# Performance work log

Measured on AMD Instinct MI355X. Metric: run time of the kernel, lower is better.

## Reference

```python
import jax, jax.numpy as jnp
import numpy as np

N_NODES = 100000
N_EDGES = 1600000
EDGES_IN = 1
HID = 64
OUT = 64


def setup_inputs() -> dict:
    key = jax.random.key(0)
    ks = jax.random.split(key, 10)
    s = lambda fan_in: 1.0 / np.sqrt(fan_in)
    inp = {
        "edge_index": jax.random.randint(ks[0], (2, N_EDGES), 0, N_NODES, dtype=jnp.int64) if jax.config.jax_enable_x64 else jax.random.randint(ks[0], (2, N_EDGES), 0, N_NODES, dtype=jnp.int32),
        "edge_attr": jax.random.normal(ks[1], (N_EDGES, EDGES_IN), dtype=jnp.float32),
        # edge MLP: Linear(EDGES_IN->HID), SiLU, Linear(HID->HID), SiLU
        "W1": jax.random.uniform(ks[2], (EDGES_IN, HID), jnp.float32, -s(EDGES_IN), s(EDGES_IN)),
        "b1": jax.random.uniform(ks[3], (HID,), jnp.float32, -s(EDGES_IN), s(EDGES_IN)),
        "W2": jax.random.uniform(ks[4], (HID, HID), jnp.float32, -s(HID), s(HID)),
        "b2": jax.random.uniform(ks[5], (HID,), jnp.float32, -s(HID), s(HID)),
        # node MLP: Linear(HID->HID), SiLU, Linear(HID->OUT)
        "W3": jax.random.uniform(ks[6], (HID, HID), jnp.float32, -s(HID), s(HID)),
        "b3": jax.random.uniform(ks[7], (HID,), jnp.float32, -s(HID), s(HID)),
        "W4": jax.random.uniform(ks[8], (HID, OUT), jnp.float32, -s(HID), s(HID)),
        "b4": jax.random.uniform(ks[9], (OUT,), jnp.float32, -s(HID), s(HID)),
    }
    return inp


def reference(edge_index, edge_attr, W1, b1, W2, b2, W3, b3, W4, b4):
    silu = jax.nn.silu
    # edge model: [E, EDGES_IN] -> [E, HID]
    ef = silu(edge_attr @ W1 + b1)
    ef = silu(ef @ W2 + b2)
    # unsorted_segment_sum over source nodes (row): [E, HID] -> [N, HID]
    row = edge_index[0]
    agg = jax.ops.segment_sum(ef, row, num_segments=N_NODES)
    # node model: [N, HID] -> [N, OUT]
    h = silu(agg @ W3 + b3) @ W4 + b4
    return h
```

## Files before the change

kernel.cpp:

```cpp
#include <hip/hip_runtime.h>
#include <math.h>
#include <utility>

#define TN 4096
#define XMIN (-8.0f)
#define XMAX (8.0f)

#define GB1 256
#define MAXBK 1024
#define S2_ELEMS 2048
#define S2_BS 256
#define BKN 128
#define BKCAP 3072

typedef __attribute__((ext_vector_type(8))) short short8;
typedef __attribute__((ext_vector_type(4))) float f32x4;

__device__ __forceinline__ float silu_f(float v) {
    return v / (1.0f + __expf(-v));
}

__device__ __forceinline__ unsigned short f2bf(float x) {
    unsigned u = __float_as_uint(x);
    return (unsigned short)((u + 0x7FFFu + ((u >> 16) & 1u)) >> 16);
}
__device__ __forceinline__ float bf2f(unsigned short h) {
    return __uint_as_float(((unsigned)h) << 16);
}

#define SPLIT8(w0,w1,w2,w3,w4,w5,w6,w7, H, L) { \
    unsigned short _h0=f2bf(w0),_h1=f2bf(w1),_h2=f2bf(w2),_h3=f2bf(w3), \
                   _h4=f2bf(w4),_h5=f2bf(w5),_h6=f2bf(w6),_h7=f2bf(w7); \
    H = (short8){(short)_h0,(short)_h1,(short)_h2,(short)_h3, \
                 (short)_h4,(short)_h5,(short)_h6,(short)_h7}; \
    L = (short8){(short)f2bf((w0)-bf2f(_h0)),(short)f2bf((w1)-bf2f(_h1)), \
                 (short)f2bf((w2)-bf2f(_h2)),(short)f2bf((w3)-bf2f(_h3)), \
                 (short)f2bf((w4)-bf2f(_h4)),(short)f2bf((w5)-bf2f(_h5)), \
                 (short)f2bf((w6)-bf2f(_h6)),(short)f2bf((w7)-bf2f(_h7))}; }

#define BFRAG(Wp, kc, nt, H, L) { \
    const float* _p = (Wp) + ((kc)*32 + quad*8)*64 + (nt)*16 + m; \
    SPLIT8(_p[0],_p[64],_p[128],_p[192],_p[256],_p[320],_p[384],_p[448], H, L) }

#define MFMA3(AH, AL, BH, BL, ACC) \
    ACC = __builtin_amdgcn_mfma_f32_16x16x32_bf16(AH, BH, ACC, 0, 0, 0); \
    ACC = __builtin_amdgcn_mfma_f32_16x16x32_bf16(AL, BH, ACC, 0, 0, 0); \
    ACC = __builtin_amdgcn_mfma_f32_16x16x32_bf16(AH, BL, ACC, 0, 0, 0);

__global__ void build_table_k(const float* __restrict__ W1, const float* __restrict__ b1,
                              const float* __restrict__ W2, const float* __restrict__ b2,
                              float* __restrict__ table) {
    int gid  = blockIdx.x * blockDim.x + threadIdx.x;
    int wave = gid >> 6;
    int lane = gid & 63;
    if (wave >= TN) return;
    const float step = (XMAX - XMIN) / (float)(TN - 1);
    float x  = XMIN + step * (float)wave;
    float h1 = silu_f(fmaf(x, W1[lane], b1[lane]));
    float acc = b2[lane];
#pragma unroll
    for (int k = 0; k < 64; ++k) {
        float h1k = __shfl(h1, k, 64);
        acc = fmaf(h1k, W2[k * 64 + lane], acc);
    }
    table[wave * 64 + lane] = silu_f(acc);
}

__global__ void bhist_k(const int* __restrict__ row, int* __restrict__ bh,
                        int E, int nbk) {
    __shared__ int h[MAXBK];
    int t = threadIdx.x;
    for (int e = t; e < nbk; e += 256) h[e] = 0;
    __syncthreads();
    for (int i = blockIdx.x * 256 + t; i < E; i += 256 * GB1)
        atomicAdd(&h[row[i] >> 7], 1);
    __syncthreads();
    for (int e = t; e < nbk; e += 256)
        bh[e * GB1 + blockIdx.x] = h[e];
}

__global__ void scan2A_k(const int* __restrict__ in, int* __restrict__ out,
                         int* __restrict__ bsum, int n) {
    __shared__ int b0[S2_ELEMS], b1[S2_ELEMS];
    int t = threadIdx.x, base = blockIdx.x * S2_ELEMS;
    for (int e = t; e < S2_ELEMS; e += S2_BS)
        b0[e] = (base + e < n) ? in[base + e] : 0;
    __syncthreads();
    int* src = b0; int* dst = b1;
    for (int d = 1; d < S2_ELEMS; d <<= 1) {
        for (int e = t; e < S2_ELEMS; e += S2_BS)
            dst[e] = src[e] + ((e >= d) ? src[e - d] : 0);
        __syncthreads();
        int* tmp = src; src = dst; dst = tmp;
    }
    for (int e = t; e < S2_ELEMS; e += S2_BS)
        if (base + e < n) out[base + e] = (e == 0) ? 0 : src[e - 1];
    if (t == 0) bsum[blockIdx.x] = src[S2_ELEMS - 1];
}

__global__ void scanB_k(int* __restrict__ bsum, int nb) {
    __shared__ int b0[256], b1[256];
    int t = threadIdx.x;
    b0[t] = (t < nb) ? bsum[t] : 0;
    __syncthreads();
    int* src = b0; int* dst = b1;
    for (int d = 1; d < 256; d <<= 1) {
        dst[t] = src[t] + ((t >= d) ? src[t - d] : 0);
        __syncthreads();
        int* tmp = src; src = dst; dst = tmp;
    }
    if (t < nb) bsum[t] = (t == 0) ? 0 : src[t - 1];
}

__global__ void scan2C_k(int* __restrict__ out, const int* __restrict__ bsum, int n) {
    int i = blockIdx.x * blockDim.x + threadIdx.x;
    if (i < n) out[i] += bsum[i >> 11];
}

__global__ void bscatter_k(const int* __restrict__ row, const float* __restrict__ x,
                           const int* __restrict__ bhs, unsigned int* __restrict__ packed,
                           int E, int nbk) {
    __shared__ int cur[MAXBK];
    int t = threadIdx.x;
    for (int e = t; e < nbk; e += 256) cur[e] = bhs[e * GB1 + blockIdx.x];
    __syncthreads();
    const float scale = (float)(TN - 1) / (XMAX - XMIN);
    for (int i = blockIdx.x * 256 + t; i < E; i += 256 * GB1) {
        int   r  = row[i];
        float xv = x[i];
        float tt = fminf(fmaxf((xv - XMIN) * scale, 0.f), (float)(TN - 1) - 0.001f);
        int   i0 = (int)tt;
        unsigned int q = min((unsigned int)((tt - (float)i0) * 8192.0f), 8191u);
        unsigned int pk = ((unsigned int)(r & 127) << 25) | ((unsigned int)i0 << 13) | q;
        int p = atomicAdd(&cur[r >> 7], 1);
        packed[p] = pk;
    }
}

__global__ __launch_bounds__(256, 8)
void gather_k(const unsigned int* __restrict__ packed, const int* __restrict__ bhs,
              const float* __restrict__ table, float* __restrict__ aggOut,
              int N, int E, int nbk) {
    __shared__ unsigned int srt[BKCAP];
    __shared__ int hist[BKN + 1];
    __shared__ int curs[BKN];
    int t = threadIdx.x, lane = t & 63, wid = t >> 6;
    int b = blockIdx.x;

    int s  = bhs[b * GB1];
    int e_ = (b + 1 < nbk) ? bhs[(b + 1) * GB1] : E;
    int cnt = min(e_ - s, BKCAP);

    for (int i = t; i <= BKN; i += 256) hist[i] = 0;
    __syncthreads();
    for (int i = t; i < cnt; i += 256)
        atomicAdd(&hist[packed[s + i] >> 25], 1);
    __syncthreads();

    if (wid == 0) {
        int c0 = hist[lane], c1 = hist[64 + lane];
        int s0 = c0, s1 = c1;
#pragma unroll
        for (int d = 1; d < 64; d <<= 1) {
            int u0 = __shfl_up(s0, d, 64);
            int u1 = __shfl_up(s1, d, 64);
            if (lane >= d) { s0 += u0; s1 += u1; }
        }
        int tot0 = __shfl(s0, 63, 64);
        hist[lane]      = s0 - c0;         curs[lane]      = s0 - c0;
        hist[64 + lane] = tot0 + s1 - c1;  curs[64 + lane] = tot0 + s1 - c1;
        if (lane == 63) hist[BKN] = tot0 + s1;
    }
    __syncthreads();

    for (int i = t; i < cnt; i += 256) {
        unsigned int p = packed[s + i];
        int pos = atomicAdd(&curs[p >> 25], 1);
        srt[pos] = p;
    }
    __syncthreads();

    for (int nl = wid; nl < BKN; nl += 4) {
        int n = (b << 7) + nl;
        if (n >= N) break;
        int beg = hist[nl], dn = hist[nl + 1] - beg;
        float a0 = 0.f, a1 = 0.f, a2 = 0.f, a3 = 0.f;
        int j = 0;
        for (; j + 4 <= dn; j += 4) {
            unsigned int p0 = srt[beg + j + 0];
            unsigned int p1 = srt[beg + j + 1];
            unsigned int p2 = srt[beg + j + 2];
            unsigned int p3 = srt[beg + j + 3];
            const float* r0 = table + (((p0 >> 13) & 0xFFFu) << 6) + lane;
            const float* r1 = table + (((p1 >> 13) & 0xFFFu) << 6) + lane;
            const float* r2 = table + (((p2 >> 13) & 0xFFFu) << 6) + lane;
            const float* r3 = table + (((p3 >> 13) & 0xFFFu) << 6) + lane;
            float u0 = r0[0], v0 = r0[64];
            float u1 = r1[0], v1 = r1[64];
            float u2 = r2[0], v2 = r2[64];
            float u3 = r3[0], v3 = r3[64];
            float f0 = (float)(p0 & 0x1FFFu) * (1.0f / 8192.0f);
            float f1 = (float)(p1 & 0x1FFFu) * (1.0f / 8192.0f);
            float f2 = (float)(p2 & 0x1FFFu) * (1.0f / 8192.0f);
            float f3 = (float)(p3 & 0x1FFFu) * (1.0f / 8192.0f);
            a0 = fmaf(f0, v0 - u0, a0 + u0);
            a1 = fmaf(f1, v1 - u1, a1 + u1);
            a2 = fmaf(f2, v2 - u2, a2 + u2);
            a3 = fmaf(f3, v3 - u3, a3 + u3);
        }
        for (; j < dn; ++j) {
            unsigned int p0 = srt[beg + j];
            const float* r0 = table + (((p0 >> 13) & 0xFFFu) << 6) + lane;
            float u0 = r0[0], v0 = r0[64];
            float f0 = (float)(p0 & 0x1FFFu) * (1.0f / 8192.0f);
            a0 = fmaf(f0, v0 - u0, a0 + u0);
        }
        aggOut[(size_t)n * 64 + lane] = (a0 + a1) + (a2 + a3);
    }
}

__global__ __launch_bounds__(256, 1)
void mlp_k(const float* __restrict__ W3, const float* __restrict__ b3,
           const float* __restrict__ W4, const float* __restrict__ b4,
           float* __restrict__ h, int N) {
    __shared__ float gt[4][16 * 68];
    int t = threadIdx.x, lane = t & 63, wid = t >> 6;
    int m = lane & 15, quad = lane >> 4;
    long r0 = (long)blockIdx.x * 64 + wid * 16;
    if (r0 >= N) return;

    short8 B3h00,B3l00,B3h01,B3l01, B3h10,B3l10,B3h11,B3l11;
    short8 B3h20,B3l20,B3h21,B3l21, B3h30,B3l30,B3h31,B3l31;
    short8 B4h00,B4l00,B4h01,B4l01, B4h10,B4l10,B4h11,B4l11;
    short8 B4h20,B4l20,B4h21,B4l21, B4h30,B4l30,B4h31,B4l31;
    BFRAG(W3, 0, 0, B3h00, B3l00)  BFRAG(W3, 1, 0, B3h01, B3l01)
    BFRAG(W3, 0, 1, B3h10, B3l10)  BFRAG(W3, 1, 1, B3h11, B3l11)
    BFRAG(W3, 0, 2, B3h20, B3l20)  BFRAG(W3, 1, 2, B3h21, B3l21)
    BFRAG(W3, 0, 3, B3h30, B3l30)  BFRAG(W3, 1, 3, B3h31, B3l31)
    BFRAG(W4, 0, 0, B4h00, B4l00)  BFRAG(W4, 1, 0, B4h01, B4l01)
    BFRAG(W4, 0, 1, B4h10, B4l10)  BFRAG(W4, 1, 1, B4h11, B4l11)
    BFRAG(W4, 0, 2, B4h20, B4l20)  BFRAG(W4, 1, 2, B4h21, B4l21)
    BFRAG(W4, 0, 3, B4h30, B4l30)  BFRAG(W4, 1, 3, B4h31, B4l31)

    long ra = r0 + m; if (ra > N - 1) ra = N - 1;
    const float* ap = h + ra * 64 + quad * 8;
    float4 p0 = *(const float4*)(ap);       float4 p1 = *(const float4*)(ap + 4);
    float4 p2 = *(const float4*)(ap + 32);  float4 p3 = *(const float4*)(ap + 36);
    short8 Ah0, Al0, Ah1, Al1;
    SPLIT8(p0.x,p0.y,p0.z,p0.w,p1.x,p1.y,p1.z,p1.w, Ah0, Al0)
    SPLIT8(p2.x,p2.y,p2.z,p2.w,p3.x,p3.y,p3.z,p3.w, Ah1, Al1)

    f32x4 acc0 = {0.f,0.f,0.f,0.f}, acc1 = {0.f,0.f,0.f,0.f};
    f32x4 acc2 = {0.f,0.f,0.f,0.f}, acc3 = {0.f,0.f,0.f,0.f};
    MFMA3(Ah0, Al0, B3h00, B3l00, acc0)  MFMA3(Ah1, Al1, B3h01, B3l01, acc0)
    MFMA3(Ah0, Al0, B3h10, B3l10, acc1)  MFMA3(Ah1, Al1, B3h11, B3l11, acc1)
    MFMA3(Ah0, Al0, B3h20, B3l20, acc2)  MFMA3(Ah1, Al1, B3h21, B3l21, acc2)
    MFMA3(Ah0, Al0, B3h30, B3l30, acc3)  MFMA3(Ah1, Al1, B3h31, B3l31, acc3)

    float* g = gt[wid];
    {
        float bv = b3[0*16 + m];
        g[(quad*4+0)*68 + 0*16 + m] = silu_f(acc0.x + bv);
        g[(quad*4+1)*68 + 0*16 + m] = silu_f(acc0.y + bv);
        g[(quad*4+2)*68 + 0*16 + m] = silu_f(acc0.z + bv);
        g[(quad*4+3)*68 + 0*16 + m] = silu_f(acc0.w + bv);
    }
    {
        float bv = b3[1*16 + m];
        g[(quad*4+0)*68 + 1*16 + m] = silu_f(acc1.x + bv);
        g[(quad*4+1)*68 + 1*16 + m] = silu_f(acc1.y + bv);
        g[(quad*4+2)*68 + 1*16 + m] = silu_f(acc1.z + bv);
        g[(quad*4+3)*68 + 1*16 + m] = silu_f(acc1.w + bv);
    }
    {
        float bv = b3[2*16 + m];
        g[(quad*4+0)*68 + 2*16 + m] = silu_f(acc2.x + bv);
        g[(quad*4+1)*68 + 2*16 + m] = silu_f(acc2.y + bv);
        g[(quad*4+2)*68 + 2*16 + m] = silu_f(acc2.z + bv);
        g[(quad*4+3)*68 + 2*16 + m] = silu_f(acc2.w + bv);
    }
    {
        float bv = b3[3*16 + m];
        g[(quad*4+0)*68 + 3*16 + m] = silu_f(acc3.x + bv);
        g[(quad*4+1)*68 + 3*16 + m] = silu_f(acc3.y + bv);
        g[(quad*4+2)*68 + 3*16 + m] = silu_f(acc3.z + bv);
        g[(quad*4+3)*68 + 3*16 + m] = silu_f(acc3.w + bv);
    }
    __syncthreads();

    const float* gp = g + m * 68 + quad * 8;
    float4 q0 = *(const float4*)(gp);       float4 q1 = *(const float4*)(gp + 4);
    float4 q2 = *(const float4*)(gp + 32);  float4 q3 = *(const float4*)(gp + 36);
    short8 Gh0, Gl0, Gh1, Gl1;
    SPLIT8(q0.x,q0.y,q0.z,q0.w,q1.x,q1.y,q1.z,q1.w, Gh0, Gl0)
    SPLIT8(q2.x,q2.y,q2.z,q2.w,q3.x,q3.y,q3.z,q3.w, Gh1, Gl1)

    f32x4 o0 = {0.f,0.f,0.f,0.f}, o1 = {0.f,0.f,0.f,0.f};
    f32x4 o2 = {0.f,0.f,0.f,0.f}, o3 = {0.f,0.f,0.f,0.f};
    MFMA3(Gh0, Gl0, B4h00, B4l00, o0)  MFMA3(Gh1, Gl1, B4h01, B4l01, o0)
    MFMA3(Gh0, Gl0, B4h10, B4l10, o1)  MFMA3(Gh1, Gl1, B4h11, B4l11, o1)
    MFMA3(Gh0, Gl0, B4h20, B4l20, o2)  MFMA3(Gh1, Gl1, B4h21, B4l21, o2)
    MFMA3(Gh0, Gl0, B4h30, B4l30, o3)  MFMA3(Gh1, Gl1, B4h31, B4l31, o3)

    long rw = r0 + quad * 4;
    float c0 = b4[0*16 + m], c1 = b4[1*16 + m], c2 = b4[2*16 + m], c3 = b4[3*16 + m];
    if (rw + 0 < N) { float* o = h + (rw+0)*64;
        o[ 0+m]=o0.x+c0; o[16+m]=o1.x+c1; o[32+m]=o2.x+c2; o[48+m]=o3.x+c3; }
    if (rw + 1 < N) { float* o = h + (rw+1)*64;
        o[ 0+m]=o0.y+c0; o[16+m]=o1.y+c1; o[32+m]=o2.y+c2; o[48+m]=o3.y+c3; }
    if (rw + 2 < N) { float* o = h + (rw+2)*64;
        o[ 0+m]=o0.z+c0; o[16+m]=o1.z+c1; o[32+m]=o2.z+c2; o[48+m]=o3.z+c3; }
    if (rw + 3 < N) { float* o = h + (rw+3)*64;
        o[ 0+m]=o0.w+c0; o[16+m]=o1.w+c1; o[32+m]=o2.w+c2; o[48+m]=o3.w+c3; }
}

__global__ void zero_k(float4* __restrict__ p, int n4) {
    int i = blockIdx.x * blockDim.x + threadIdx.x;
    int stride = gridDim.x * blockDim.x;
    float4 z = make_float4(0.f, 0.f, 0.f, 0.f);
    for (; i < n4; i += stride) p[i] = z;
}

__global__ void edge_k(const int* __restrict__ row, const float* __restrict__ xarr,
                       const float* __restrict__ table, float* __restrict__ agg, int E) {
    int gid    = blockIdx.x * blockDim.x + threadIdx.x;
    int lane   = gid & 63;
    int wave   = gid >> 6;
    int nwaves = (gridDim.x * blockDim.x) >> 6;
    const float scale = (float)(TN - 1) / (XMAX - XMIN);
    for (int e = wave; e < E; e += nwaves) {
        float x = xarr[e];
        int   r = row[e];
        float t = fminf(fmaxf((x - XMIN) * scale, 0.0f), (float)(TN - 1) - 0.001f);
        int   i0 = (int)t;
        float f  = t - (float)i0;
        const float* tp = table + (size_t)i0 * 64 + lane;
        float v0 = tp[0];
        float v1 = tp[64];
        atomicAdd(agg + (size_t)r * 64 + lane, fmaf(f, v1 - v0, v0));
    }
}

extern "C" void kernel_launch(void* const* d_in, const int* in_sizes, int n_in,
                              void* d_out, int out_size, void* d_ws, size_t ws_size,
                              hipStream_t stream) {
    const int*   edge_index = (const int*)  d_in[0];
    const float* edge_attr  = (const float*)d_in[1];
    const float* W1 = (const float*)d_in[2];
    const float* b1 = (const float*)d_in[3];
    const float* W2 = (const float*)d_in[4];
    const float* b2 = (const float*)d_in[5];
    const float* W3 = (const float*)d_in[6];
    const float* b3 = (const float*)d_in[7];
    const float* W4 = (const float*)d_in[8];
    const float* b4 = (const float*)d_in[9];

    float* out = (float*)d_out;
    const int E   = in_sizes[1];
    const int N   = out_size / 64;
    const int nbk = (N + 127) >> 7;
    const int M   = nbk * GB1;
    const int nsb = (M + S2_ELEMS - 1) / S2_ELEMS;
    const int nmb = (N + 63) / 64;

    char* ws = (char*)d_ws;
    size_t off = 0;
    auto carve = [&](size_t bytes) { size_t r = off; off = (off + bytes + 255) & ~(size_t)255; return r; };
    size_t tableOff = carve((size_t)TN * 64 * 4);
    size_t bhOff    = carve((size_t)M * 4);
    size_t bsumOff  = carve((size_t)nsb * 4);
    size_t pkOff    = carve((size_t)E * 4);
    bool fits = (off <= ws_size) && (nbk <= MAXBK) && (nsb <= 256);

    float* table = (float*)(ws + tableOff);

    build_table_k<<<TN / 4, 256, 0, stream>>>(W1, b1, W2, b2, table);

    if (fits) {
        int* bh   = (int*)(ws + bhOff);
        int* bsum = (int*)(ws + bsumOff);
        unsigned int* packed = (unsigned int*)(ws + pkOff);

        bhist_k  <<<GB1, 256, 0, stream>>>(edge_index, bh, E, nbk);
        scan2A_k <<<nsb, S2_BS, 0, stream>>>(bh, bh, bsum, M);
        scanB_k  <<<1, 256, 0, stream>>>(bsum, nsb);
        scan2C_k <<<(M + 255) / 256, 256, 0, stream>>>(bh, bsum, M);
        bscatter_k<<<GB1, 256, 0, stream>>>(edge_index, edge_attr, bh, packed, E, nbk);
        gather_k <<<nbk, 256, 0, stream>>>(packed, bh, table, out, N, E, nbk);
        mlp_k    <<<nmb, 256, 0, stream>>>(W3, b3, W4, b4, out, N);
    } else {
        zero_k<<<4096, 256, 0, stream>>>((float4*)out, (N * 64) / 4);
        edge_k<<<8192, 256, 0, stream>>>(edge_index, edge_attr, table, out, E);
        mlp_k <<<nmb, 256, 0, stream>>>(W3, b3, W4, b4, out, N);
    }
}
```

Before: 211.3 us.

## Simplify bucket sort pipeline, halve bucket size, interleave table, prepack MLP weights

Replaces the per-block histogram matrix and three-kernel scan with global atomic bucket counts plus a single-block scan. Bucket scatter positions are now reserved per block with atomics, at a staggered bucket order. Buckets shrink from 128 to 64 nodes, giving twice as many gather blocks with smaller shared staging. The lookup table is stored with adjacent entries interleaved so each lane fetches both interpolation points in one float2 load. MLP weight fragments are split into bf16 hi/lo once in a separate kernel instead of in every block. Together these cut launch count and redundant work, at the cost of global atomics and a different scatter order.

```diff
diff --git a/kernel.cpp b/kernel.cpp
--- a/kernel.cpp
+++ b/kernel.cpp
@@ -7,11 +7,9 @@
 #define XMAX (8.0f)
 
 #define GB1 256
-#define MAXBK 1024
-#define S2_ELEMS 2048
-#define S2_BS 256
-#define BKN 128
-#define BKCAP 3072
+#define MAXBK 2048
+#define BKN 64
+#define BKCAP 1792
 
 typedef __attribute__((ext_vector_type(8))) short short8;
 typedef __attribute__((ext_vector_type(4))) float f32x4;
@@ -49,8 +47,9 @@
 
 __global__ void build_table_k(const float* __restrict__ W1, const float* __restrict__ b1,
                               const float* __restrict__ W2, const float* __restrict__ b2,
-                              float* __restrict__ table) {
+                              float* __restrict__ table2, int* __restrict__ cnt, int nbk) {
     int gid  = blockIdx.x * blockDim.x + threadIdx.x;
+    if (gid < nbk) cnt[gid] = 0;
     int wave = gid >> 6;
     int lane = gid & 63;
     if (wave >= TN) return;
@@ -63,66 +62,75 @@
         float h1k = __shfl(h1, k, 64);
         acc = fmaf(h1k, W2[k * 64 + lane], acc);
     }
-    table[wave * 64 + lane] = silu_f(acc);
-}
-
-__global__ void bhist_k(const int* __restrict__ row, int* __restrict__ bh,
+    float val = silu_f(acc);
+    table2[(size_t)wave * 128 + 2 * lane] = val;
+    if (wave > 0)
+        table2[(size_t)(wave - 1) * 128 + 2 * lane + 1] = val;
+}
+
+__global__ void pack_w_k(const float* __restrict__ W3, const float* __restrict__ W4,
+                         short8* __restrict__ packW) {
+    int t = threadIdx.x, lane = t & 63, wid = t >> 6;
+    int m = lane & 15, quad = lane >> 4;
+    for (int f = wid; f < 16; f += 4) {
+        const float* Wp = (f < 8) ? W3 : W4;
+        int kc = f & 1, nt = (f >> 1) & 3;
+        short8 H, L;
+        BFRAG(Wp, kc, nt, H, L)
+        packW[(2 * f + 0) * 64 + lane] = H;
+        packW[(2 * f + 1) * 64 + lane] = L;
+    }
+}
+
+__global__ void bhist_k(const int* __restrict__ row, int* __restrict__ cnt,
                         int E, int nbk) {
     __shared__ int h[MAXBK];
     int t = threadIdx.x;
     for (int e = t; e < nbk; e += 256) h[e] = 0;
     __syncthreads();
     for (int i = blockIdx.x * 256 + t; i < E; i += 256 * GB1)
-        atomicAdd(&h[row[i] >> 7], 1);
+        atomicAdd(&h[row[i] >> 6], 1);
     __syncthreads();
     for (int e = t; e < nbk; e += 256)
-        bh[e * GB1 + blockIdx.x] = h[e];
-}
-
-__global__ void scan2A_k(const int* __restrict__ in, int* __restrict__ out,
-                         int* __restrict__ bsum, int n) {
-    __shared__ int b0[S2_ELEMS], b1[S2_ELEMS];
-    int t = threadIdx.x, base = blockIdx.x * S2_ELEMS;
-    for (int e = t; e < S2_ELEMS; e += S2_BS)
-        b0[e] = (base + e < n) ? in[base + e] : 0;
+        if (h[e]) atomicAdd(&cnt[e], h[e]);
+}
+
+__global__ void scan1_k(const int* __restrict__ cnt, int* __restrict__ bhs,
+                        int* __restrict__ cur, int n) {
+    __shared__ int b0[MAXBK], b1[MAXBK];
+    int t = threadIdx.x;
+    for (int e = t; e < MAXBK; e += 1024) b0[e] = (e < n) ? cnt[e] : 0;
     __syncthreads();
     int* src = b0; int* dst = b1;
-    for (int d = 1; d < S2_ELEMS; d <<= 1) {
-        for (int e = t; e < S2_ELEMS; e += S2_BS)
+    for (int d = 1; d < MAXBK; d <<= 1) {
+        for (int e = t; e < MAXBK; e += 1024)
             dst[e] = src[e] + ((e >= d) ? src[e - d] : 0);
         __syncthreads();
         int* tmp = src; src = dst; dst = tmp;
     }
-    for (int e = t; e < S2_ELEMS; e += S2_BS)
-        if (base + e < n) out[base + e] = (e == 0) ? 0 : src[e - 1];
-    if (t == 0) bsum[blockIdx.x] = src[S2_ELEMS - 1];
-}
-
-__global__ void scanB_k(int* __restrict__ bsum, int nb) {
-    __shared__ int b0[256], b1[256];
+    for (int e = t; e < n; e += 1024) {
+        int v = (e == 0) ? 0 : src[e - 1];
+        bhs[e] = v; cur[e] = v;
+    }
+    if (t == 0) bhs[n] = src[n - 1];
+}
+
+__global__ void bscatter_k(const int* __restrict__ row, const float* __restrict__ x,
+                           int* __restrict__ cur, unsigned int* __restrict__ packed,
+                           int E, int nbk) {
+    __shared__ int hist[MAXBK];
     int t = threadIdx.x;
-    b0[t] = (t < nb) ? bsum[t] : 0;
-    __syncthreads();
-    int* src = b0; int* dst = b1;
-    for (int d = 1; d < 256; d <<= 1) {
-        dst[t] = src[t] + ((t >= d) ? src[t - d] : 0);
-        __syncthreads();
-        int* tmp = src; src = dst; dst = tmp;
-    }
-    if (t < nb) bsum[t] = (t == 0) ? 0 : src[t - 1];
-}
-
-__global__ void scan2C_k(int* __restrict__ out, const int* __restrict__ bsum, int n) {
-    int i = blockIdx.x * blockDim.x + threadIdx.x;
-    if (i < n) out[i] += bsum[i >> 11];
-}
-
-__global__ void bscatter_k(const int* __restrict__ row, const float* __restrict__ x,
-                           const int* __restrict__ bhs, unsigned int* __restrict__ packed,
-                           int E, int nbk) {
-    __shared__ int cur[MAXBK];
-    int t = threadIdx.x;
-    for (int e = t; e < nbk; e += 256) cur[e] = bhs[e * GB1 + blockIdx.x];
+    for (int e = t; e < nbk; e += 256) hist[e] = 0;
+    __syncthreads();
+    for (int i = blockIdx.x * 256 + t; i < E; i += 256 * GB1)
+        atomicAdd(&hist[row[i] >> 6], 1);
+    __syncthreads();
+    int shift = (int)(((long)blockIdx.x * nbk) >> 8);
+    for (int k = t; k < nbk; k += 256) {
+        int e = k + shift; if (e >= nbk) e -= nbk;
+        int c = hist[e];
+        hist[e] = c ? atomicAdd(&cur[e], c) : 0;
+    }
     __syncthreads();
     const float scale = (float)(TN - 1) / (XMAX - XMIN);
     for (int i = blockIdx.x * 256 + t; i < E; i += 256 * GB1) {
@@ -131,24 +139,23 @@
         float tt = fminf(fmaxf((xv - XMIN) * scale, 0.f), (float)(TN - 1) - 0.001f);
         int   i0 = (int)tt;
         unsigned int q = min((unsigned int)((tt - (float)i0) * 8192.0f), 8191u);
-        unsigned int pk = ((unsigned int)(r & 127) << 25) | ((unsigned int)i0 << 13) | q;
-        int p = atomicAdd(&cur[r >> 7], 1);
+        unsigned int pk = ((unsigned int)(r & 63) << 25) | ((unsigned int)i0 << 13) | q;
+        int p = atomicAdd(&hist[r >> 6], 1);
         packed[p] = pk;
     }
 }
 
 __global__ __launch_bounds__(256, 8)
 void gather_k(const unsigned int* __restrict__ packed, const int* __restrict__ bhs,
-              const float* __restrict__ table, float* __restrict__ aggOut,
-              int N, int E, int nbk) {
+              const float* __restrict__ table2, float* __restrict__ aggOut, int N) {
     __shared__ unsigned int srt[BKCAP];
     __shared__ int hist[BKN + 1];
     __shared__ int curs[BKN];
     int t = threadIdx.x, lane = t & 63, wid = t >> 6;
     int b = blockIdx.x;
 
-    int s  = bhs[b * GB1];
-    int e_ = (b + 1 < nbk) ? bhs[(b + 1) * GB1] : E;
+    int s   = bhs[b];
+    int e_  = bhs[b + 1];
     int cnt = min(e_ - s, BKCAP);
 
     for (int i = t; i <= BKN; i += 256) hist[i] = 0;
@@ -158,18 +165,15 @@
     __syncthreads();
 
     if (wid == 0) {
-        int c0 = hist[lane], c1 = hist[64 + lane];
-        int s0 = c0, s1 = c1;
+        int c = hist[lane];
+        int sc = c;
 #pragma unroll
         for (int d = 1; d < 64; d <<= 1) {
-            int u0 = __shfl_up(s0, d, 64);
-            int u1 = __shfl_up(s1, d, 64);
-            if (lane >= d) { s0 += u0; s1 += u1; }
+            int u = __shfl_up(sc, d, 64);
+            if (lane >= d) sc += u;
         }
-        int tot0 = __shfl(s0, 63, 64);
-        hist[lane]      = s0 - c0;         curs[lane]      = s0 - c0;
-        hist[64 + lane] = tot0 + s1 - c1;  curs[64 + lane] = tot0 + s1 - c1;
-        if (lane == 63) hist[BKN] = tot0 + s1;
+        hist[lane] = sc - c;  curs[lane] = sc - c;
+        if (lane == 63) hist[BKN] = sc;
     }
     __syncthreads();
 
@@ -180,8 +184,9 @@
     }
     __syncthreads();
 
+    const float2* tab = (const float2*)table2 + lane;
     for (int nl = wid; nl < BKN; nl += 4) {
-        int n = (b << 7) + nl;
+        int n = (b << 6) + nl;
         if (n >= N) break;
         int beg = hist[nl], dn = hist[nl + 1] - beg;
         float a0 = 0.f, a1 = 0.f, a2 = 0.f, a3 = 0.f;
@@ -191,56 +196,49 @@
             unsigned int p1 = srt[beg + j + 1];
             unsigned int p2 = srt[beg + j + 2];
             unsigned int p3 = srt[beg + j + 3];
-            const float* r0 = table + (((p0 >> 13) & 0xFFFu) << 6) + lane;
-            const float* r1 = table + (((p1 >> 13) & 0xFFFu) << 6) + lane;
-            const float* r2 = table + (((p2 >> 13) & 0xFFFu) << 6) + lane;
-            const float* r3 = table + (((p3 >> 13) & 0xFFFu) << 6) + lane;
-            float u0 = r0[0], v0 = r0[64];
-            float u1 = r1[0], v1 = r1[64];
-            float u2 = r2[0], v2 = r2[64];
-            float u3 = r3[0], v3 = r3[64];
+            float2 uv0 = tab[(p0 >> 7) & 0x3FFC0u];
+            float2 uv1 = tab[(p1 >> 7) & 0x3FFC0u];
+            float2 uv2 = tab[(p2 >> 7) & 0x3FFC0u];
+            float2 uv3 = tab[(p3 >> 7) & 0x3FFC0u];
             float f0 = (float)(p0 & 0x1FFFu) * (1.0f / 8192.0f);
             float f1 = (float)(p1 & 0x1FFFu) * (1.0f / 8192.0f);
             float f2 = (float)(p2 & 0x1FFFu) * (1.0f / 8192.0f);
             float f3 = (float)(p3 & 0x1FFFu) * (1.0f / 8192.0f);
-            a0 = fmaf(f0, v0 - u0, a0 + u0);
-            a1 = fmaf(f1, v1 - u1, a1 + u1);
-            a2 = fmaf(f2, v2 - u2, a2 + u2);
-            a3 = fmaf(f3, v3 - u3, a3 + u3);
+            a0 = fmaf(f0, uv0.y - uv0.x, a0 + uv0.x);
+            a1 = fmaf(f1, uv1.y - uv1.x, a1 + uv1.x);
+            a2 = fmaf(f2, uv2.y - uv2.x, a2 + uv2.x);
+            a3 = fmaf(f3, uv3.y - uv3.x, a3 + uv3.x);
         }
         for (; j < dn; ++j) {
             unsigned int p0 = srt[beg + j];
-            const float* r0 = table + (((p0 >> 13) & 0xFFFu) << 6) + lane;
-            float u0 = r0[0], v0 = r0[64];
+            float2 uv0 = tab[(p0 >> 7) & 0x3FFC0u];
             float f0 = (float)(p0 & 0x1FFFu) * (1.0f / 8192.0f);
-            a0 = fmaf(f0, v0 - u0, a0 + u0);
+            a0 = fmaf(f0, uv0.y - uv0.x, a0 + uv0.x);
         }
         aggOut[(size_t)n * 64 + lane] = (a0 + a1) + (a2 + a3);
     }
 }
 
 __global__ __launch_bounds__(256, 1)
-void mlp_k(const float* __restrict__ W3, const float* __restrict__ b3,
-           const float* __restrict__ W4, const float* __restrict__ b4,
-           float* __restrict__ h, int N) {
+void mlp_k(const short8* __restrict__ packW, const float* __restrict__ b3,
+           const float* __restrict__ b4, float* __restrict__ h, int N) {
     __shared__ float gt[4][16 * 68];
     int t = threadIdx.x, lane = t & 63, wid = t >> 6;
     int m = lane & 15, quad = lane >> 4;
     long r0 = (long)blockIdx.x * 64 + wid * 16;
     if (r0 >= N) return;
 
-    short8 B3h00,B3l00,B3h01,B3l01, B3h10,B3l10,B3h11,B3l11;
-    short8 B3h20,B3l20,B3h21,B3l21, B3h30,B3l30,B3h31,B3l31;
-    short8 B4h00,B4l00,B4h01,B4l01, B4h10,B4l10,B4h11,B4l11;
-    short8 B4h20,B4l20,B4h21,B4l21, B4h30,B4l30,B4h31,B4l31;
-    BFRAG(W3, 0, 0, B3h00, B3l00)  BFRAG(W3, 1, 0, B3h01, B3l01)
-    BFRAG(W3, 0, 1, B3h10, B3l10)  BFRAG(W3, 1, 1, B3h11, B3l11)
-    BFRAG(W3, 0, 2, B3h20, B3l20)  BFRAG(W3, 1, 2, B3h21, B3l21)
-    BFRAG(W3, 0, 3, B3h30, B3l30)  BFRAG(W3, 1, 3, B3h31, B3l31)
-    BFRAG(W4, 0, 0, B4h00, B4l00)  BFRAG(W4, 1, 0, B4h01, B4l01)
-    BFRAG(W4, 0, 1, B4h10, B4l10)  BFRAG(W4, 1, 1, B4h11, B4l11)
-    BFRAG(W4, 0, 2, B4h20, B4l20)  BFRAG(W4, 1, 2, B4h21, B4l21)
-    BFRAG(W4, 0, 3, B4h30, B4l30)  BFRAG(W4, 1, 3, B4h31, B4l31)
+    const short8* pw = packW + lane;
+#define LDW(s) pw[(s) * 64]
+    short8 B3h00=LDW( 0), B3l00=LDW( 1), B3h01=LDW( 2), B3l01=LDW( 3);
+    short8 B3h10=LDW( 4), B3l10=LDW( 5), B3h11=LDW( 6), B3l11=LDW( 7);
+    short8 B3h20=LDW( 8), B3l20=LDW( 9), B3h21=LDW(10), B3l21=LDW(11);
+    short8 B3h30=LDW(12), B3l30=LDW(13), B3h31=LDW(14), B3l31=LDW(15);
+    short8 B4h00=LDW(16), B4l00=LDW(17), B4h01=LDW(18), B4l01=LDW(19);
+    short8 B4h10=LDW(20), B4l10=LDW(21), B4h11=LDW(22), B4l11=LDW(23);
+    short8 B4h20=LDW(24), B4l20=LDW(25), B4h21=LDW(26), B4l21=LDW(27);
+    short8 B4h30=LDW(28), B4l30=LDW(29), B4h31=LDW(30), B4l31=LDW(31);
+#undef LDW
 
     long ra = r0 + m; if (ra > N - 1) ra = N - 1;
     const float* ap = h + ra * 64 + quad * 8;
@@ -322,22 +320,21 @@
 }
 
 __global__ void edge_k(const int* __restrict__ row, const float* __restrict__ xarr,
-                       const float* __restrict__ table, float* __restrict__ agg, int E) {
+                       const float* __restrict__ table2, float* __restrict__ agg, int E) {
     int gid    = blockIdx.x * blockDim.x + threadIdx.x;
     int lane   = gid & 63;
     int wave   = gid >> 6;
     int nwaves = (gridDim.x * blockDim.x) >> 6;
     const float scale = (float)(TN - 1) / (XMAX - XMIN);
+    const float2* tab = (const float2*)table2 + lane;
     for (int e = wave; e < E; e += nwaves) {
         float x = xarr[e];
         int   r = row[e];
         float t = fminf(fmaxf((x - XMIN) * scale, 0.0f), (float)(TN - 1) - 0.001f);
         int   i0 = (int)t;
         float f  = t - (float)i0;
-        const float* tp = table + (size_t)i0 * 64 + lane;
-        float v0 = tp[0];
-        float v1 = tp[64];
-        atomicAdd(agg + (size_t)r * 64 + lane, fmaf(f, v1 - v0, v0));
+        float2 uv = tab[i0 << 6];
+        atomicAdd(agg + (size_t)r * 64 + lane, fmaf(f, uv.y - uv.x, uv.x));
     }
 }
 
@@ -358,39 +355,41 @@
     float* out = (float*)d_out;
     const int E   = in_sizes[1];
     const int N   = out_size / 64;
-    const int nbk = (N + 127) >> 7;
-    const int M   = nbk * GB1;
-    const int nsb = (M + S2_ELEMS - 1) / S2_ELEMS;
+    const int nbk = (N + 63) >> 6;
     const int nmb = (N + 63) / 64;
 
     char* ws = (char*)d_ws;
     size_t off = 0;
     auto carve = [&](size_t bytes) { size_t r = off; off = (off + bytes + 255) & ~(size_t)255; return r; };
-    size_t tableOff = carve((size_t)TN * 64 * 4);
-    size_t bhOff    = carve((size_t)M * 4);
-    size_t bsumOff  = carve((size_t)nsb * 4);
+    size_t tableOff = carve((size_t)TN * 128 * 4);
+    size_t packWOff = carve((size_t)32 * 64 * 16);
+    size_t cntOff   = carve((size_t)nbk * 4);
+    size_t bhsOff   = carve((size_t)(nbk + 1) * 4);
+    size_t curOff   = carve((size_t)nbk * 4);
     size_t pkOff    = carve((size_t)E * 4);
-    bool fits = (off <= ws_size) && (nbk <= MAXBK) && (nsb <= 256);
-
-    float* table = (float*)(ws + tableOff);
-
-    build_table_k<<<TN / 4, 256, 0, stream>>>(W1, b1, W2, b2, table);
+    bool fits = (off <= ws_size) && (nbk <= MAXBK);
+
+    float*  table2 = (float*)(ws + tableOff);
+    short8* packW  = (short8*)(ws + packWOff);
+    int*    cnt    = (int*)(ws + cntOff);
+
+    build_table_k<<<TN / 4, 256, 0, stream>>>(W1, b1, W2, b2, table2, cnt,
+                                              fits ? nbk : 0);
+    pack_w_k<<<1, 256, 0, stream>>>(W3, W4, packW);
 
     if (fits) {
-        int* bh   = (int*)(ws + bhOff);
-        int* bsum = (int*)(ws + bsumOff);
+        int* bhs = (int*)(ws + bhsOff);
+        int* cur = (int*)(ws + curOff);
         unsigned int* packed = (unsigned int*)(ws + pkOff);
 
-        bhist_k  <<<GB1, 256, 0, stream>>>(edge_index, bh, E, nbk);
-        scan2A_k <<<nsb, S2_BS, 0, stream>>>(bh, bh, bsum, M);
-        scanB_k  <<<1, 256, 0, stream>>>(bsum, nsb);
-        scan2C_k <<<(M + 255) / 256, 256, 0, stream>>>(bh, bsum, M);
-        bscatter_k<<<GB1, 256, 0, stream>>>(edge_index, edge_attr, bh, packed, E, nbk);
-        gather_k <<<nbk, 256, 0, stream>>>(packed, bh, table, out, N, E, nbk);
-        mlp_k    <<<nmb, 256, 0, stream>>>(W3, b3, W4, b4, out, N);
+        bhist_k   <<<GB1, 256, 0, stream>>>(edge_index, cnt, E, nbk);
+        scan1_k   <<<1, 1024, 0, stream>>>(cnt, bhs, cur, nbk);
+        bscatter_k<<<GB1, 256, 0, stream>>>(edge_index, edge_attr, cur, packed, E, nbk);
+        gather_k  <<<nbk, 256, 0, stream>>>(packed, bhs, table2, out, N);
+        mlp_k     <<<nmb, 256, 0, stream>>>(packW, b3, b4, out, N);
     } else {
         zero_k<<<4096, 256, 0, stream>>>((float4*)out, (N * 64) / 4);
-        edge_k<<<8192, 256, 0, stream>>>(edge_index, edge_attr, table, out, E);
-        mlp_k <<<nmb, 256, 0, stream>>>(W3, b3, W4, b4, out, N);
-    }
-}
+        edge_k<<<8192, 256, 0, stream>>>(edge_index, edge_attr, table2, out, E);
+        mlp_k <<<nmb, 256, 0, stream>>>(packW, b3, b4, out, N);
+    }
+}
```

Measured after the change: 210.8 us. Within noise of the previous version (-0.3%).
